# Performance work log

Measured on AMD Instinct MI355X. Metric: run time of the kernel, lower is better.

Reference implementation:

```python
import jax, jax.numpy as jnp
import numpy as np

D_MODEL = 1024
LAYER_IDX = 5
D_FF = 4096
SPARSITY = 0.9
TOKENS = 8192
IN_UP = D_MODEL * (LAYER_IDX + 1)  # 6144


def _sparse_weight(rng, out_f, in_f, sparsity):
    """Row-wise k-sparse weight matrix mimicking SparseLinear's padded-CSR:
    each output row keeps k = round(in_f*(1-sparsity)) live columns,
    values ~ U(-b, b) with b = 1/sqrt(effective_fan_in)."""
    k = max(1, round(in_f * (1.0 - sparsity)))
    bound = 1.0 / np.sqrt(max(1.0, in_f * (1.0 - sparsity)))
    scores = rng.random((out_f, in_f))
    # top-k per row -> boolean mask
    thresh = np.partition(scores, in_f - k, axis=1)[:, in_f - k][:, None]
    mask = scores >= thresh
    W = (rng.uniform(-bound, bound, (out_f, in_f)).astype(np.float32)) * mask
    return jnp.asarray(W), jnp.asarray(mask)


def setup_inputs() -> dict:
    key = jax.random.key(0)
    x = jax.random.normal(key, (TOKENS, IN_UP), dtype=jnp.float32)
    rng = np.random.default_rng(0)
    W_up, mask_up = _sparse_weight(rng, D_FF, IN_UP, SPARSITY)
    W_down, mask_down = _sparse_weight(rng, D_MODEL, D_FF, SPARSITY)
    return {"ffn_input_cat": x, "W_up": W_up, "W_down": W_down,
            "mask_up": mask_up, "mask_down": mask_down}


def reference(ffn_input_cat, W_up, W_down, mask_up, mask_down):
    # fc_down(gelu(fc_up(x))); SparseLinear == masked dense linear, no bias.
    # torch F.gelu default is the exact (erf) gelu.
    h = jax.nn.gelu(ffn_input_cat @ (W_up * mask_up).T, approximate=False)  # [T, d_ff]
    return h @ (W_down * mask_down).T  # [T, d_model]
```

## Files before the change

### kernel.cpp

```cpp
#include <hip/hip_runtime.h>
#include <cstdint>
#include <cstddef>

typedef unsigned short u16;
typedef __attribute__((ext_vector_type(8))) short  bf16x8;
typedef __attribute__((ext_vector_type(4))) float  f32x4;

__device__ __forceinline__ u16 f2bf(float f) {
    unsigned u = __float_as_uint(f);
    unsigned r = (u + 0x7FFFu + ((u >> 16) & 1u)) >> 16;
    return (u16)r;
}

__device__ __forceinline__ void async_lds16(const u16* g, u16* l) {
    __builtin_amdgcn_global_load_lds(
        (const __attribute__((address_space(1))) unsigned int*)g,
        (__attribute__((address_space(3))) unsigned int*)l,
        16, 0, 0);
}

__global__ __launch_bounds__(256) void cvt3_kernel(const float* __restrict__ s0, u16* __restrict__ d0, int n0,
                                                   const float* __restrict__ s1, u16* __restrict__ d1, int n1,
                                                   const float* __restrict__ s2, u16* __restrict__ d2, int n2) {
    int i = blockIdx.x * 256 + threadIdx.x;
    const float* s; u16* d;
    if (i < n0)            { s = s0; d = d0; }
    else if (i < n0 + n1)  { s = s1; d = d1; i -= n0; }
    else                   { s = s2; d = d2; i -= n0 + n1; if (i >= n2) return; }
    const float4* sp = (const float4*)s;
    float4 a = sp[2 * i];
    float4 b = sp[2 * i + 1];
    union { bf16x8 v; u16 e[8]; } o;
    o.e[0] = f2bf(a.x); o.e[1] = f2bf(a.y); o.e[2] = f2bf(a.z); o.e[3] = f2bf(a.w);
    o.e[4] = f2bf(b.x); o.e[5] = f2bf(b.y); o.e[6] = f2bf(b.z); o.e[7] = f2bf(b.w);
    ((bf16x8*)d)[i] = o.v;
}

#define KHSZ (256 * 32)

template<bool GELU, typename OutT>
__global__ __launch_bounds__(512, 2) void gemm256(const u16* __restrict__ A,
                                                  const u16* __restrict__ B,
                                                  OutT* __restrict__ C,
                                                  int K, int lda, int ldb, int ldc) {
    __shared__ __align__(16) u16 sA[2][2][KHSZ];
    __shared__ __align__(16) u16 sB[2][2][KHSZ];

    const int tid  = threadIdx.x;
    const int wave = tid >> 6;
    const int lane = tid & 63;
    const int quad = lane >> 4;
    const int r16  = lane & 15;

    const int nwg = gridDim.x * gridDim.y;
    int lin = blockIdx.y * gridDim.x + blockIdx.x;
    lin = (lin & 7) * (nwg >> 3) + (lin >> 3);
    const int n0 = (lin % gridDim.x) * 256;
    const int m0 = (lin / gridDim.x) * 256;

    const int wm = (wave >> 2) * 128;
    const int wn = (wave & 3) * 64;

    const int srow = tid >> 2;
    const int scol = ((tid & 3) ^ ((srow >> 1) & 3)) * 8;
    const int ld0  = (wave * 16) * 32;
    const int ld1  = (128 + wave * 16) * 32;

    const u16* gA0 = A + (size_t)(m0 + srow) * lda + scol;
    const u16* gA1 = A + (size_t)(m0 + 128 + srow) * lda + scol;
    const u16* gB0 = B + (size_t)(n0 + srow) * ldb + scol;
    const u16* gB1 = B + (size_t)(n0 + 128 + srow) * ldb + scol;

#define STAGE_A(t, kh) { const int ko_ = (t) * 64 + (kh) * 32; u16* d_ = &sA[(t) & 1][kh][0]; \
        async_lds16(gA0 + ko_, d_ + ld0); async_lds16(gA1 + ko_, d_ + ld1); }
#define STAGE_B(t, kh) { const int ko_ = (t) * 64 + (kh) * 32; u16* d_ = &sB[(t) & 1][kh][0]; \
        async_lds16(gB0 + ko_, d_ + ld0); async_lds16(gB1 + ko_, d_ + ld1); }

    int oA[8], oB[4];
#pragma unroll
    for (int i = 0; i < 8; i++) {
        int ra = wm + i * 16 + r16;
        oA[i] = ra * 32 + ((quad ^ ((ra >> 1) & 3)) << 3);
    }
#pragma unroll
    for (int i = 0; i < 4; i++) {
        int rb = wn + i * 16 + r16;
        oB[i] = rb * 32 + ((quad ^ ((rb >> 1) & 3)) << 3);
    }

    f32x4 acc[8][4] = {};
    const int NT = K / 64;

    STAGE_A(0, 0); STAGE_B(0, 0); STAGE_A(0, 1); STAGE_B(0, 1);
    STAGE_A(1, 0); STAGE_B(1, 0);
    asm volatile("s_waitcnt vmcnt(4)" ::: "memory");
    __builtin_amdgcn_s_barrier();

#define MFMA16(mbase, AF, BF) \
    __builtin_amdgcn_s_barrier(); \
    asm volatile("s_waitcnt lgkmcnt(0)" ::: "memory"); \
    __builtin_amdgcn_sched_barrier(0); \
    __builtin_amdgcn_s_setprio(1); \
    _Pragma("unroll") \
    for (int mi_ = 0; mi_ < 4; mi_++) \
        _Pragma("unroll") \
        for (int ni_ = 0; ni_ < 4; ni_++) \
            acc[(mbase) + mi_][ni_] = __builtin_amdgcn_mfma_f32_16x16x32_bf16( \
                AF[mi_], BF[ni_], acc[(mbase) + mi_][ni_], 0, 0, 0); \
    __builtin_amdgcn_s_setprio(0); \
    __builtin_amdgcn_sched_barrier(0);

    for (int t = 0; t < NT; ++t) {
        const u16* At0 = &sA[t & 1][0][0];
        const u16* At1 = &sA[t & 1][1][0];
        const u16* Bt0 = &sB[t & 1][0][0];
        const u16* Bt1 = &sB[t & 1][1][0];
        const int tn  = (t + 1 < NT) ? t + 1 : t + 1 - NT;
        const int tn2 = (t + 2 < NT) ? t + 2 : t + 2 - NT;

        bf16x8 af[4], bf[4];

#pragma unroll
        for (int i = 0; i < 4; i++) {
            af[i] = *(const bf16x8*)&At0[oA[i]];
            bf[i] = *(const bf16x8*)&Bt0[oB[i]];
        }
        STAGE_A(tn, 1); STAGE_B(tn, 1);
        MFMA16(0, af, bf);
        __builtin_amdgcn_s_barrier();

#pragma unroll
        for (int i = 0; i < 4; i++) af[i] = *(const bf16x8*)&At0[oA[4 + i]];
        MFMA16(4, af, bf);
        __builtin_amdgcn_s_barrier();

#pragma unroll
        for (int i = 0; i < 4; i++) {
            af[i] = *(const bf16x8*)&At1[oA[i]];
            bf[i] = *(const bf16x8*)&Bt1[oB[i]];
        }
        STAGE_A(tn2, 0); STAGE_B(tn2, 0);
        MFMA16(0, af, bf);
        __builtin_amdgcn_s_barrier();

#pragma unroll
        for (int i = 0; i < 4; i++) af[i] = *(const bf16x8*)&At1[oA[4 + i]];
        MFMA16(4, af, bf);
        asm volatile("s_waitcnt vmcnt(4)" ::: "memory");
        __builtin_amdgcn_s_barrier();
    }

#pragma unroll
    for (int mi = 0; mi < 8; mi++) {
#pragma unroll
        for (int r = 0; r < 4; r++) {
            size_t rowoff = (size_t)(m0 + wm + mi * 16 + quad * 4 + r) * ldc;
#pragma unroll
            for (int ni = 0; ni < 4; ni++) {
                int col = n0 + wn + ni * 16 + r16;
                float v = acc[mi][ni][r];
                if constexpr (GELU)
                    v = 0.5f * v * (1.0f + erff(v * 0.70710678118654752f));
                if constexpr (sizeof(OutT) == 2)
                    ((u16*)C)[rowoff + col] = f2bf(v);
                else
                    ((float*)C)[rowoff + col] = v;
            }
        }
    }
}

extern "C" void kernel_launch(void* const* d_in, const int* in_sizes, int n_in,
                              void* d_out, int out_size, void* d_ws, size_t ws_size,
                              hipStream_t stream) {
    const int T   = 8192;
    const int DIN = 6144;
    const int DFF = 4096;
    const int DM  = 1024;

    const float* x  = (const float*)d_in[0];
    const float* wu = (const float*)d_in[1];
    const float* wd = (const float*)d_in[2];

    u16* xb  = (u16*)d_ws;
    u16* wub = xb  + (size_t)T * DIN;
    u16* wdb = wub + (size_t)DFF * DIN;
    u16* hb  = wdb + (size_t)DM * DFF;

    const int n8x  = T * DIN / 8;
    const int n8wu = DFF * DIN / 8;
    const int n8wd = DM * DFF / 8;
    cvt3_kernel<<<(n8x + n8wu + n8wd) / 256, 256, 0, stream>>>(
        x, xb, n8x, wu, wub, n8wu, wd, wdb, n8wd);

    dim3 g1(DFF / 256, T / 256);
    gemm256<true, u16><<<g1, 512, 0, stream>>>(xb, wub, hb, DIN, DIN, DIN, DFF);

    dim3 g2(DM / 256, T / 256);
    gemm256<false, float><<<g2, 512, 0, stream>>>(hb, wdb, (float*)d_out,
                                                  DFF, DFF, DFF, DM);
}
```

Before: 939.2 us.

## Double-buffer LDS fragment loads in GEMM mainloop and grid-stride the convert kernel

The GEMM inner loop now keeps two register sets of A/B fragments, so the LDS reads for the next MFMA quarter are issued while the current quarter's MFMAs run. This also removes several per-quarter barriers. The first fragments of the next K tile are prefetched before the last MFMA block. The fp32-to-bf16 conversion kernel becomes a grid-stride loop over float4 elements with a fixed grid of 8192 blocks. In exchange, fragment register pressure goes up, and the reworked waitcnt/barrier ordering has to stay correct.

```diff
diff --git a/kernel.cpp b/kernel.cpp
--- a/kernel.cpp
+++ b/kernel.cpp
@@ -5,6 +5,7 @@
 typedef unsigned short u16;
 typedef __attribute__((ext_vector_type(8))) short  bf16x8;
 typedef __attribute__((ext_vector_type(4))) float  f32x4;
+typedef __attribute__((ext_vector_type(4))) unsigned short u16x4;
 
 __device__ __forceinline__ u16 f2bf(float f) {
     unsigned u = __float_as_uint(f);
@@ -22,18 +23,17 @@
 __global__ __launch_bounds__(256) void cvt3_kernel(const float* __restrict__ s0, u16* __restrict__ d0, int n0,
                                                    const float* __restrict__ s1, u16* __restrict__ d1, int n1,
                                                    const float* __restrict__ s2, u16* __restrict__ d2, int n2) {
-    int i = blockIdx.x * 256 + threadIdx.x;
-    const float* s; u16* d;
-    if (i < n0)            { s = s0; d = d0; }
-    else if (i < n0 + n1)  { s = s1; d = d1; i -= n0; }
-    else                   { s = s2; d = d2; i -= n0 + n1; if (i >= n2) return; }
-    const float4* sp = (const float4*)s;
-    float4 a = sp[2 * i];
-    float4 b = sp[2 * i + 1];
-    union { bf16x8 v; u16 e[8]; } o;
-    o.e[0] = f2bf(a.x); o.e[1] = f2bf(a.y); o.e[2] = f2bf(a.z); o.e[3] = f2bf(a.w);
-    o.e[4] = f2bf(b.x); o.e[5] = f2bf(b.y); o.e[6] = f2bf(b.z); o.e[7] = f2bf(b.w);
-    ((bf16x8*)d)[i] = o.v;
+    const int total = n0 + n1 + n2;
+    for (int i = blockIdx.x * 256 + threadIdx.x; i < total; i += gridDim.x * 256) {
+        const float* s; u16* d; int j = i;
+        if (j < n0)            { s = s0; d = d0; }
+        else if (j < n0 + n1)  { s = s1; d = d1; j -= n0; }
+        else                   { s = s2; d = d2; j -= n0 + n1; }
+        float4 a = ((const float4*)s)[j];
+        u16x4 o;
+        o[0] = f2bf(a.x); o[1] = f2bf(a.y); o[2] = f2bf(a.z); o[3] = f2bf(a.w);
+        ((u16x4*)d)[j] = o;
+    }
 }
 
 #define KHSZ (256 * 32)
@@ -91,15 +91,9 @@
     f32x4 acc[8][4] = {};
     const int NT = K / 64;
 
-    STAGE_A(0, 0); STAGE_B(0, 0); STAGE_A(0, 1); STAGE_B(0, 1);
-    STAGE_A(1, 0); STAGE_B(1, 0);
-    asm volatile("s_waitcnt vmcnt(4)" ::: "memory");
-    __builtin_amdgcn_s_barrier();
-
-#define MFMA16(mbase, AF, BF) \
-    __builtin_amdgcn_s_barrier(); \
-    asm volatile("s_waitcnt lgkmcnt(0)" ::: "memory"); \
-    __builtin_amdgcn_sched_barrier(0); \
+#define LGKM0 asm volatile("s_waitcnt lgkmcnt(0)" ::: "memory"); __builtin_amdgcn_sched_barrier(0)
+#define SBAR  __builtin_amdgcn_sched_barrier(0)
+#define MFMA_Q(mbase, AF, BF) \
     __builtin_amdgcn_s_setprio(1); \
     _Pragma("unroll") \
     for (int mi_ = 0; mi_ < 4; mi_++) \
@@ -108,46 +102,70 @@
             acc[(mbase) + mi_][ni_] = __builtin_amdgcn_mfma_f32_16x16x32_bf16( \
                 AF[mi_], BF[ni_], acc[(mbase) + mi_][ni_], 0, 0, 0); \
     __builtin_amdgcn_s_setprio(0); \
-    __builtin_amdgcn_sched_barrier(0);
+    __builtin_amdgcn_sched_barrier(0)
+
+    bf16x8 afA[4], afB[4], bfA[4], bfB[4];
+
+    STAGE_A(0, 0); STAGE_B(0, 0);
+    STAGE_A(0, 1); STAGE_B(0, 1);
+    STAGE_A(1, 0); STAGE_B(1, 0);
+    asm volatile("s_waitcnt vmcnt(4)" ::: "memory");
+    __builtin_amdgcn_s_barrier();
+    SBAR;
+    {
+        const u16* Ak0 = &sA[0][0][0];
+        const u16* Bk0 = &sB[0][0][0];
+#pragma unroll
+        for (int i = 0; i < 4; i++) {
+            afA[i] = *(const bf16x8*)&Ak0[oA[i]];
+            bfA[i] = *(const bf16x8*)&Bk0[oB[i]];
+        }
+    }
 
     for (int t = 0; t < NT; ++t) {
-        const u16* At0 = &sA[t & 1][0][0];
-        const u16* At1 = &sA[t & 1][1][0];
-        const u16* Bt0 = &sB[t & 1][0][0];
-        const u16* Bt1 = &sB[t & 1][1][0];
+        const u16* Ak0 = &sA[t & 1][0][0];
+        const u16* Ak1 = &sA[t & 1][1][0];
+        const u16* Bk1 = &sB[t & 1][1][0];
+        const u16* nAk0 = &sA[(t + 1) & 1][0][0];
+        const u16* nBk0 = &sB[(t + 1) & 1][0][0];
         const int tn  = (t + 1 < NT) ? t + 1 : t + 1 - NT;
         const int tn2 = (t + 2 < NT) ? t + 2 : t + 2 - NT;
 
-        bf16x8 af[4], bf[4];
-
+        LGKM0;
+        STAGE_A(tn, 1); STAGE_B(tn, 1);
+#pragma unroll
+        for (int i = 0; i < 4; i++) afB[i] = *(const bf16x8*)&Ak0[oA[4 + i]];
+        SBAR;
+        MFMA_Q(0, afA, bfA);
+
+        LGKM0;
 #pragma unroll
         for (int i = 0; i < 4; i++) {
-            af[i] = *(const bf16x8*)&At0[oA[i]];
-            bf[i] = *(const bf16x8*)&Bt0[oB[i]];
-        }
-        STAGE_A(tn, 1); STAGE_B(tn, 1);
-        MFMA16(0, af, bf);
+            afA[i] = *(const bf16x8*)&Ak1[oA[i]];
+            bfB[i] = *(const bf16x8*)&Bk1[oB[i]];
+        }
+        SBAR;
+        MFMA_Q(4, afB, bfA);
+
         __builtin_amdgcn_s_barrier();
-
-#pragma unroll
-        for (int i = 0; i < 4; i++) af[i] = *(const bf16x8*)&At0[oA[4 + i]];
-        MFMA16(4, af, bf);
-        __builtin_amdgcn_s_barrier();
-
-#pragma unroll
-        for (int i = 0; i < 4; i++) {
-            af[i] = *(const bf16x8*)&At1[oA[i]];
-            bf[i] = *(const bf16x8*)&Bt1[oB[i]];
-        }
+        LGKM0;
         STAGE_A(tn2, 0); STAGE_B(tn2, 0);
-        MFMA16(0, af, bf);
-        __builtin_amdgcn_s_barrier();
-
-#pragma unroll
-        for (int i = 0; i < 4; i++) af[i] = *(const bf16x8*)&At1[oA[4 + i]];
-        MFMA16(4, af, bf);
+#pragma unroll
+        for (int i = 0; i < 4; i++) afB[i] = *(const bf16x8*)&Ak1[oA[4 + i]];
+        SBAR;
+        MFMA_Q(0, afA, bfB);
+
+        LGKM0;
         asm volatile("s_waitcnt vmcnt(4)" ::: "memory");
         __builtin_amdgcn_s_barrier();
+        SBAR;
+#pragma unroll
+        for (int i = 0; i < 4; i++) {
+            afA[i] = *(const bf16x8*)&nAk0[oA[i]];
+            bfA[i] = *(const bf16x8*)&nBk0[oB[i]];
+        }
+        SBAR;
+        MFMA_Q(4, afB, bfB);
     }
 
 #pragma unroll
@@ -187,11 +205,10 @@
     u16* wdb = wub + (size_t)DFF * DIN;
     u16* hb  = wdb + (size_t)DM * DFF;
 
-    const int n8x  = T * DIN / 8;
-    const int n8wu = DFF * DIN / 8;
-    const int n8wd = DM * DFF / 8;
-    cvt3_kernel<<<(n8x + n8wu + n8wd) / 256, 256, 0, stream>>>(
-        x, xb, n8x, wu, wub, n8wu, wd, wdb, n8wd);
+    const int n4x  = T * DIN / 4;
+    const int n4wu = DFF * DIN / 4;
+    const int n4wd = DM * DFF / 4;
+    cvt3_kernel<<<8192, 256, 0, stream>>>(x, xb, n4x, wu, wub, n4wu, wd, wdb, n4wd);
 
     dim3 g1(DFF / 256, T / 256);
     gemm256<true, u16><<<g1, 512, 0, stream>>>(xb, wub, hb, DIN, DIN, DIN, DFF);
```

Result: no change. 955.1 us (+1.7%).
